# Kernel tuning notes

Measured on AMD Instinct MI355X. Metric: run time of the kernel, lower is better.

The kernel has to match this reference:

```python
import jax, jax.numpy as jnp
import numpy as np

NTOKENS = 50257
NHID = 1024
NPC = int(np.ceil(np.sqrt(NTOKENS)))            # 225 tokens per class
NCLASSES = int(np.ceil(NTOKENS / NPC))          # 224 classes
BATCH = 1024
INITRANGE = 0.1


def setup_inputs() -> dict:
    key = jax.random.key(0)
    k1, k2, k3, k4 = jax.random.split(key, 4)
    inputs = jax.random.normal(k1, (BATCH, NHID), dtype=jnp.float32)
    labels = jax.random.randint(k2, (BATCH,), 0, NTOKENS, dtype=jnp.int64)
    layer_top_W = jax.random.uniform(k3, (NHID, NCLASSES), minval=-INITRANGE, maxval=INITRANGE, dtype=jnp.float32)
    layer_top_b = jnp.zeros((NCLASSES,), dtype=jnp.float32)
    layer_bottom_W = jax.random.uniform(k4, (NCLASSES, NHID, NPC), minval=-INITRANGE, maxval=INITRANGE, dtype=jnp.float32)
    layer_bottom_b = jnp.zeros((NCLASSES, NPC), dtype=jnp.float32)
    return {
        "inputs": inputs,
        "labels": labels,
        "layer_top_W": layer_top_W,
        "layer_top_b": layer_top_b,
        "layer_bottom_W": layer_bottom_W,
        "layer_bottom_b": layer_bottom_b,
    }


def reference(inputs, labels, layer_top_W, layer_top_b, layer_bottom_W, layer_bottom_b):
    batch_size = inputs.shape[0]
    # decompose label into (class, within-class) position; old-torch `/` on Long == floor div
    pos_top = labels // NPC            # [B]
    pos_bottom = labels % NPC          # [B]

    # top-level class distribution: [B, nclasses]
    top_logits = inputs @ layer_top_W + layer_top_b
    top_probs = jax.nn.softmax(top_logits, axis=1)

    # gather per-sample class weight slices and do batched matvec:
    # layer_bottom_W[pos_top]: [B, nhid, npc]
    bottom_logits = jnp.einsum("bd,bdc->bc", inputs, layer_bottom_W[pos_top]) + layer_bottom_b[pos_top]
    bottom_probs = jax.nn.softmax(bottom_logits, axis=1)

    rows = jnp.arange(batch_size)
    target_probs = top_probs[rows, pos_top] * bottom_probs[rows, pos_bottom]  # [B]
    return target_probs
```

## Files before the change

kernel.cpp:

```cpp
#include <hip/hip_runtime.h>
#include <math.h>

#define NHID 1024
#define NPC  225
#define NCLS 224
#define BATCH 1024

#define MAX_ITEMS 352
#define N_TOP     (BATCH / 8)

#define WS_NITEMS 0
#define WS_ORDER  16
#define WS_ITEMS  2048
#define WS_PTOP   4096

__device__ __forceinline__ void group_samples(const int* __restrict__ labels,
                                              int* __restrict__ ws,
                                              float* __restrict__ smf, int tid)
{
    int* cnt   = (int*)smf;
    int* scan  = (int*)smf + 256;
    int* iscan = (int*)smf + 512;
    int* cur   = (int*)smf + 768;

    if (tid < 256) cnt[tid] = 0;
    __syncthreads();
    for (int i = tid; i < BATCH; i += 1024)
        atomicAdd(&cnt[labels[i] / NPC], 1);
    __syncthreads();

    int myc = 0, myi = 0;
    if (tid < 256) {
        myc = (tid < NCLS) ? cnt[tid] : 0;
        myi = (myc + 7) >> 3;
        scan[tid]  = myc;
        iscan[tid] = myi;
    }
    __syncthreads();
    for (int off = 1; off < 256; off <<= 1) {
        int a = 0, b = 0;
        if (tid < 256 && tid >= off) { a = scan[tid - off]; b = iscan[tid - off]; }
        __syncthreads();
        if (tid < 256) { scan[tid] += a; iscan[tid] += b; }
        __syncthreads();
    }
    if (tid < 256) {
        const int sbase = scan[tid]  - myc;
        const int ibase = iscan[tid] - myi;
        if (tid == 255) ws[WS_NITEMS] = iscan[255];
        cur[tid] = sbase;
        if (tid < NCLS) {
            for (int t = 0; t < myi; ++t) {
                int* it = ws + WS_ITEMS + 4 * (ibase + t);
                it[0] = tid;
                it[1] = sbase + 8 * t;
                it[2] = min(8, myc - 8 * t);
            }
        }
    }
    __syncthreads();
    for (int i = tid; i < BATCH; i += 1024) {
        int c = labels[i] / NPC;
        int p = atomicAdd(&cur[c], 1);
        ws[WS_ORDER + p] = i;
    }
}

__global__ __launch_bounds__(1024, 4) void k1_top(const float* __restrict__ X,
                                                  const int* __restrict__ labels,
                                                  const float* __restrict__ Wt,
                                                  const float* __restrict__ bt,
                                                  int* __restrict__ ws)
{
    __shared__ __align__(16) float sm[14848];
    const int tid  = threadIdx.x;
    const int wave = tid >> 6;
    const int lane = tid & 63;

    if (blockIdx.x == N_TOP) {
        group_samples(labels, ws, sm, tid);
        return;
    }
    const int sbase = blockIdx.x * 8;

    for (int idx = tid; idx < 2048; idx += 1024) {
        const int j  = idx & 7;
        const int d4 = idx >> 3;
        const float4 v = ((const float4*)&X[(size_t)(sbase + j) * NHID])[d4];
        float* p = &sm[48 * d4 + j];
        p[0] = v.x; p[12] = v.y; p[24] = v.z; p[36] = v.w;
    }
    __syncthreads();

    float acc[8][4];
#pragma unroll
    for (int j = 0; j < 8; ++j)
#pragma unroll
        for (int k = 0; k < 4; ++k) acc[j][k] = 0.f;

    const int c0 = lane, c1 = lane + 64, c2 = lane + 128, c3 = lane + 192;
    const bool m3 = (c3 < NCLS);
    const int d0 = wave * 64;
    const float* Wr = Wt + (size_t)d0 * NCLS;

    auto ldrow = [&](int r, float* o) {
        const float* p = Wr + (size_t)r * NCLS;
        o[0] = p[c0]; o[1] = p[c1]; o[2] = p[c2];
        o[3] = m3 ? p[c3] : 0.f;
    };
    float wbuf[4][4];
    ldrow(0, wbuf[0]); ldrow(1, wbuf[1]); ldrow(2, wbuf[2]); ldrow(3, wbuf[3]);

#pragma unroll 4
    for (int dd = 0; dd < 64; ++dd) {
        const int slot = dd & 3;
        const float cw0 = wbuf[slot][0], cw1 = wbuf[slot][1],
                    cw2 = wbuf[slot][2], cw3 = wbuf[slot][3];
        ldrow(min(dd + 4, 63), wbuf[slot]);
        const float4 a = *(const float4*)&sm[(d0 + dd) * 12 + 0];
        const float4 b = *(const float4*)&sm[(d0 + dd) * 12 + 4];
        const float xi[8] = {a.x, a.y, a.z, a.w, b.x, b.y, b.z, b.w};
#pragma unroll
        for (int j = 0; j < 8; ++j) {
            acc[j][0] = fmaf(xi[j], cw0, acc[j][0]);
            acc[j][1] = fmaf(xi[j], cw1, acc[j][1]);
            acc[j][2] = fmaf(xi[j], cw2, acc[j][2]);
            acc[j][3] = fmaf(xi[j], cw3, acc[j][3]);
        }
    }
    __syncthreads();

    float* red = sm;
    if (wave >= 8) {
#pragma unroll
        for (int j = 0; j < 8; ++j)
#pragma unroll
            for (int k = 0; k < 4; ++k) {
                int c = lane + 64 * k;
                if (c < NCLS) red[((wave - 8) * 8 + j) * 232 + c] = acc[j][k];
            }
    }
    __syncthreads();
    if (wave < 8) {
#pragma unroll
        for (int j = 0; j < 8; ++j)
#pragma unroll
            for (int k = 0; k < 4; ++k) {
                int c = lane + 64 * k;
                if (c < NCLS) red[(wave * 8 + j) * 232 + c] += acc[j][k];
            }
    }
    __syncthreads();

    if (wave < 8) {
        const int j = wave;
        const int s = sbase + j;
        float v[4];
#pragma unroll
        for (int k = 0; k < 4; ++k) {
            int c = lane + 64 * k;
            if (c < NCLS) {
                float t = bt[c];
#pragma unroll
                for (int g = 0; g < 8; ++g) t += red[(g * 8 + j) * 232 + c];
                v[k] = t;
            } else v[k] = -INFINITY;
        }
        float m = fmaxf(fmaxf(v[0], v[1]), fmaxf(v[2], v[3]));
        for (int o = 32; o > 0; o >>= 1) m = fmaxf(m, __shfl_xor(m, o));
        float e = expf(v[0] - m) + expf(v[1] - m) + expf(v[2] - m) + expf(v[3] - m);
        for (int o = 32; o > 0; o >>= 1) e += __shfl_xor(e, o);
        const int pt = labels[s] / NPC;
        if (lane == (pt & 63))
            ((float*)(ws + WS_PTOP))[s] = expf(v[pt >> 6] - m) / e;
    }
}

__global__ __launch_bounds__(1024, 4) void k2_bottom(const float* __restrict__ X,
                                                     const int* __restrict__ labels,
                                                     const float* __restrict__ Wb,
                                                     const float* __restrict__ bb,
                                                     const int* __restrict__ ws,
                                                     float* __restrict__ out)
{
    __shared__ __align__(16) float sm[14848];
    const int nitems = ws[WS_NITEMS];
    if ((int)blockIdx.x >= nitems) return;
    const int* it = ws + WS_ITEMS + 4 * blockIdx.x;
    const int cls = it[0], s0 = it[1], nt = it[2];

    const int tid  = threadIdx.x;
    const int wave = tid >> 6;
    const int lane = tid & 63;

    int s_ids[8];
#pragma unroll
    for (int j = 0; j < 8; ++j)
        s_ids[j] = (j < nt) ? ws[WS_ORDER + s0 + j] : 0;

    for (int idx = tid; idx < 2048; idx += 1024) {
        const int j  = idx & 7;
        const int d4 = idx >> 3;
        float4 v = make_float4(0.f, 0.f, 0.f, 0.f);
        if (j < nt) v = ((const float4*)&X[(size_t)s_ids[j] * NHID])[d4];
        float* p = &sm[48 * d4 + j];
        p[0] = v.x; p[12] = v.y; p[24] = v.z; p[36] = v.w;
    }
    __syncthreads();

    float acc[8][4];
#pragma unroll
    for (int j = 0; j < 8; ++j)
#pragma unroll
        for (int k = 0; k < 4; ++k) acc[j][k] = 0.f;

    const int c0 = lane, c1 = lane + 64, c2 = lane + 128, c3 = lane + 192;
    const bool m3 = (c3 < NPC);
    const int d0 = wave * 64;
    const float* Wr = Wb + (size_t)cls * (NHID * NPC) + (size_t)d0 * NPC;

    auto ldrow = [&](int r, float* o) {
        const float* p = Wr + (size_t)r * NPC;
        o[0] = __builtin_nontemporal_load(p + c0);
        o[1] = __builtin_nontemporal_load(p + c1);
        o[2] = __builtin_nontemporal_load(p + c2);
        o[3] = m3 ? __builtin_nontemporal_load(p + c3) : 0.f;
    };
    float wbuf[4][4];
    ldrow(0, wbuf[0]); ldrow(1, wbuf[1]); ldrow(2, wbuf[2]); ldrow(3, wbuf[3]);

#pragma unroll 4
    for (int dd = 0; dd < 64; ++dd) {
        const int slot = dd & 3;
        const float cw0 = wbuf[slot][0], cw1 = wbuf[slot][1],
                    cw2 = wbuf[slot][2], cw3 = wbuf[slot][3];
        ldrow(min(dd + 4, 63), wbuf[slot]);
        const float4 a = *(const float4*)&sm[(d0 + dd) * 12 + 0];
        const float4 b = *(const float4*)&sm[(d0 + dd) * 12 + 4];
        const float xi[8] = {a.x, a.y, a.z, a.w, b.x, b.y, b.z, b.w};
#pragma unroll
        for (int j = 0; j < 8; ++j) {
            acc[j][0] = fmaf(xi[j], cw0, acc[j][0]);
            acc[j][1] = fmaf(xi[j], cw1, acc[j][1]);
            acc[j][2] = fmaf(xi[j], cw2, acc[j][2]);
            acc[j][3] = fmaf(xi[j], cw3, acc[j][3]);
        }
    }
    __syncthreads();

    float* red = sm;
    if (wave >= 8) {
#pragma unroll
        for (int j = 0; j < 8; ++j)
#pragma unroll
            for (int k = 0; k < 4; ++k) {
                int c = lane + 64 * k;
                if (c < NPC) red[((wave - 8) * 8 + j) * 232 + c] = acc[j][k];
            }
    }
    __syncthreads();
    if (wave < 8) {
#pragma unroll
        for (int j = 0; j < 8; ++j)
#pragma unroll
            for (int k = 0; k < 4; ++k) {
                int c = lane + 64 * k;
                if (c < NPC) red[(wave * 8 + j) * 232 + c] += acc[j][k];
            }
    }
    __syncthreads();

    if (wave < 8) {
        const int j = wave;
        if (j < nt) {
            const int s = s_ids[j];
            float v[4];
#pragma unroll
            for (int k = 0; k < 4; ++k) {
                int c = lane + 64 * k;
                if (c < NPC) {
                    float t = bb[(size_t)cls * NPC + c];
#pragma unroll
                    for (int g = 0; g < 8; ++g) t += red[(g * 8 + j) * 232 + c];
                    v[k] = t;
                } else v[k] = -INFINITY;
            }
            float m = fmaxf(fmaxf(v[0], v[1]), fmaxf(v[2], v[3]));
            for (int o = 32; o > 0; o >>= 1) m = fmaxf(m, __shfl_xor(m, o));
            float e = expf(v[0] - m) + expf(v[1] - m) + expf(v[2] - m) + expf(v[3] - m);
            for (int o = 32; o > 0; o >>= 1) e += __shfl_xor(e, o);
            const int pb = labels[s] % NPC;
            if (lane == (pb & 63)) {
                const float pt = ((const float*)(ws + WS_PTOP))[s];
                out[s] = pt * (expf(v[pb >> 6] - m) / e);
            }
        }
    }
}

extern "C" void kernel_launch(void* const* d_in, const int* in_sizes, int n_in,
                              void* d_out, int out_size, void* d_ws, size_t ws_size,
                              hipStream_t stream)
{
    const float* X      = (const float*)d_in[0];
    const int*   labels = (const int*)  d_in[1];
    const float* Wt     = (const float*)d_in[2];
    const float* bt     = (const float*)d_in[3];
    const float* Wb     = (const float*)d_in[4];
    const float* bb     = (const float*)d_in[5];

    hipLaunchKernelGGL(k1_top, dim3(N_TOP + 1), dim3(1024), 0, stream,
                       X, labels, Wt, bt, (int*)d_ws);
    hipLaunchKernelGGL(k2_bottom, dim3(MAX_ITEMS), dim3(1024), 0, stream,
                       X, labels, Wb, bb, (const int*)d_ws, (float*)d_out);
}
```

Measured before the change: 303.7 us.

## Fuse top and per-class bottom passes into one kernel, finalize with tiny multiply

```diff
diff --git a/kernel.cpp b/kernel.cpp
--- a/kernel.cpp
+++ b/kernel.cpp
@@ -5,89 +5,152 @@
 #define NPC  225
 #define NCLS 224
 #define BATCH 1024
-
-#define MAX_ITEMS 352
-#define N_TOP     (BATCH / 8)
-
-#define WS_NITEMS 0
-#define WS_ORDER  16
-#define WS_ITEMS  2048
-#define WS_PTOP   4096
-
-__device__ __forceinline__ void group_samples(const int* __restrict__ labels,
-                                              int* __restrict__ ws,
-                                              float* __restrict__ smf, int tid)
-{
-    int* cnt   = (int*)smf;
-    int* scan  = (int*)smf + 256;
-    int* iscan = (int*)smf + 512;
-    int* cur   = (int*)smf + 768;
-
-    if (tid < 256) cnt[tid] = 0;
-    __syncthreads();
-    for (int i = tid; i < BATCH; i += 1024)
-        atomicAdd(&cnt[labels[i] / NPC], 1);
-    __syncthreads();
-
-    int myc = 0, myi = 0;
-    if (tid < 256) {
-        myc = (tid < NCLS) ? cnt[tid] : 0;
-        myi = (myc + 7) >> 3;
-        scan[tid]  = myc;
-        iscan[tid] = myi;
-    }
-    __syncthreads();
-    for (int off = 1; off < 256; off <<= 1) {
-        int a = 0, b = 0;
-        if (tid < 256 && tid >= off) { a = scan[tid - off]; b = iscan[tid - off]; }
-        __syncthreads();
-        if (tid < 256) { scan[tid] += a; iscan[tid] += b; }
-        __syncthreads();
-    }
-    if (tid < 256) {
-        const int sbase = scan[tid]  - myc;
-        const int ibase = iscan[tid] - myi;
-        if (tid == 255) ws[WS_NITEMS] = iscan[255];
-        cur[tid] = sbase;
-        if (tid < NCLS) {
-            for (int t = 0; t < myi; ++t) {
-                int* it = ws + WS_ITEMS + 4 * (ibase + t);
-                it[0] = tid;
-                it[1] = sbase + 8 * t;
-                it[2] = min(8, myc - 8 * t);
-            }
-        }
-    }
-    __syncthreads();
-    for (int i = tid; i < BATCH; i += 1024) {
-        int c = labels[i] / NPC;
-        int p = atomicAdd(&cur[c], 1);
-        ws[WS_ORDER + p] = i;
-    }
-}
-
-__global__ __launch_bounds__(1024, 4) void k1_top(const float* __restrict__ X,
-                                                  const int* __restrict__ labels,
-                                                  const float* __restrict__ Wt,
-                                                  const float* __restrict__ bt,
-                                                  int* __restrict__ ws)
+#define N_TOP (BATCH / 8)
+
+#define WS_PT 0
+#define WS_PB 1024
+
+__global__ __launch_bounds__(1024, 4) void k_fused(const float* __restrict__ X,
+                                                   const int* __restrict__ labels,
+                                                   const float* __restrict__ Wt,
+                                                   const float* __restrict__ bt,
+                                                   const float* __restrict__ Wb,
+                                                   const float* __restrict__ bb,
+                                                   float* __restrict__ ws)
 {
     __shared__ __align__(16) float sm[14848];
+    __shared__ int slist[128];
+    __shared__ int scnt;
+
     const int tid  = threadIdx.x;
     const int wave = tid >> 6;
     const int lane = tid & 63;
-
-    if (blockIdx.x == N_TOP) {
-        group_samples(labels, ws, sm, tid);
+    const int j8   = tid & 7;
+    const int t8   = tid >> 3;
+
+    if ((int)blockIdx.x < NCLS) {
+        const int cls = blockIdx.x;
+        if (tid == 0) scnt = 0;
+        __syncthreads();
+        {
+            const int lab = labels[tid];
+            if (lab / NPC == cls) {
+                const int p = atomicAdd(&scnt, 1);
+                if (p < 128) slist[p] = tid;
+            }
+        }
+        __syncthreads();
+        const int cnt = scnt;
+        if (cnt == 0) return;
+
+        const int c0 = lane, c1 = lane + 64, c2 = lane + 128, c3 = lane + 192;
+        const bool m3 = (c3 < NPC);
+        const int d0 = wave * 64;
+        const float* Wr = Wb + (size_t)cls * (NHID * NPC) + (size_t)d0 * NPC;
+
+        for (int base = 0; base < cnt; base += 8) {
+            const int nt = min(8, cnt - base);
+
+            const int sid = (j8 < nt) ? slist[base + j8] : -1;
+            for (int d4 = t8; d4 < 256; d4 += 128) {
+                float4 v = make_float4(0.f, 0.f, 0.f, 0.f);
+                if (sid >= 0) v = ((const float4*)&X[(size_t)sid * NHID])[d4];
+                float* p = &sm[48 * d4 + j8];
+                p[0] = v.x; p[12] = v.y; p[24] = v.z; p[36] = v.w;
+            }
+            __syncthreads();
+
+            float acc[8][4];
+#pragma unroll
+            for (int j = 0; j < 8; ++j)
+#pragma unroll
+                for (int k = 0; k < 4; ++k) acc[j][k] = 0.f;
+
+            auto ldrow = [&](int r, float* o) {
+                const float* p = Wr + (size_t)r * NPC;
+                o[0] = __builtin_nontemporal_load(p + c0);
+                o[1] = __builtin_nontemporal_load(p + c1);
+                o[2] = __builtin_nontemporal_load(p + c2);
+                o[3] = m3 ? __builtin_nontemporal_load(p + c3) : 0.f;
+            };
+            float wbuf[4][4];
+            ldrow(0, wbuf[0]); ldrow(1, wbuf[1]); ldrow(2, wbuf[2]); ldrow(3, wbuf[3]);
+
+#pragma unroll 4
+            for (int dd = 0; dd < 64; ++dd) {
+                const int slot = dd & 3;
+                const float cw0 = wbuf[slot][0], cw1 = wbuf[slot][1],
+                            cw2 = wbuf[slot][2], cw3 = wbuf[slot][3];
+                ldrow(min(dd + 4, 63), wbuf[slot]);
+                const float4 a = *(const float4*)&sm[(d0 + dd) * 12 + 0];
+                const float4 b = *(const float4*)&sm[(d0 + dd) * 12 + 4];
+                const float xi[8] = {a.x, a.y, a.z, a.w, b.x, b.y, b.z, b.w};
+#pragma unroll
+                for (int j = 0; j < 8; ++j) {
+                    acc[j][0] = fmaf(xi[j], cw0, acc[j][0]);
+                    acc[j][1] = fmaf(xi[j], cw1, acc[j][1]);
+                    acc[j][2] = fmaf(xi[j], cw2, acc[j][2]);
+                    acc[j][3] = fmaf(xi[j], cw3, acc[j][3]);
+                }
+            }
+            __syncthreads();
+
+            float* red = sm;
+            if (wave >= 8) {
+#pragma unroll
+                for (int j = 0; j < 8; ++j)
+#pragma unroll
+                    for (int k = 0; k < 4; ++k) {
+                        int c = lane + 64 * k;
+                        if (c < NPC) red[((wave - 8) * 8 + j) * 232 + c] = acc[j][k];
+                    }
+            }
+            __syncthreads();
+            if (wave < 8) {
+#pragma unroll
+                for (int j = 0; j < 8; ++j)
+#pragma unroll
+                    for (int k = 0; k < 4; ++k) {
+                        int c = lane + 64 * k;
+                        if (c < NPC) red[(wave * 8 + j) * 232 + c] += acc[j][k];
+                    }
+            }
+            __syncthreads();
+
+            if (wave < 8) {
+                const int j = wave;
+                if (j < nt) {
+                    const int s = slist[base + j];
+                    float v[4];
+#pragma unroll
+                    for (int k = 0; k < 4; ++k) {
+                        int c = lane + 64 * k;
+                        if (c < NPC) {
+                            float t = bb[(size_t)cls * NPC + c];
+#pragma unroll
+                            for (int g = 0; g < 8; ++g) t += red[(g * 8 + j) * 232 + c];
+                            v[k] = t;
+                        } else v[k] = -INFINITY;
+                    }
+                    float m = fmaxf(fmaxf(v[0], v[1]), fmaxf(v[2], v[3]));
+                    for (int o = 32; o > 0; o >>= 1) m = fmaxf(m, __shfl_xor(m, o));
+                    float e = expf(v[0] - m) + expf(v[1] - m) + expf(v[2] - m) + expf(v[3] - m);
+                    for (int o = 32; o > 0; o >>= 1) e += __shfl_xor(e, o);
+                    const int pb = labels[s] % NPC;
+                    if (lane == (pb & 63))
+                        ws[WS_PB + s] = expf(v[pb >> 6] - m) / e;
+                }
+            }
+            __syncthreads();
+        }
         return;
     }
-    const int sbase = blockIdx.x * 8;
-
-    for (int idx = tid; idx < 2048; idx += 1024) {
-        const int j  = idx & 7;
-        const int d4 = idx >> 3;
-        const float4 v = ((const float4*)&X[(size_t)(sbase + j) * NHID])[d4];
-        float* p = &sm[48 * d4 + j];
+
+    const int sbase = (blockIdx.x - NCLS) * 8;
+
+    for (int d4 = t8; d4 < 256; d4 += 128) {
+        const float4 v = ((const float4*)&X[(size_t)(sbase + j8) * NHID])[d4];
+        float* p = &sm[48 * d4 + j8];
         p[0] = v.x; p[12] = v.y; p[24] = v.z; p[36] = v.w;
     }
     __syncthreads();
@@ -172,130 +235,14 @@
         for (int o = 32; o > 0; o >>= 1) e += __shfl_xor(e, o);
         const int pt = labels[s] / NPC;
         if (lane == (pt & 63))
-            ((float*)(ws + WS_PTOP))[s] = expf(v[pt >> 6] - m) / e;
+            ws[WS_PT + s] = expf(v[pt >> 6] - m) / e;
     }
 }
 
-__global__ __launch_bounds__(1024, 4) void k2_bottom(const float* __restrict__ X,
-                                                     const int* __restrict__ labels,
-                                                     const float* __restrict__ Wb,
-                                                     const float* __restrict__ bb,
-                                                     const int* __restrict__ ws,
-                                                     float* __restrict__ out)
+__global__ void k_mul(const float* __restrict__ ws, float* __restrict__ out)
 {
-    __shared__ __align__(16) float sm[14848];
-    const int nitems = ws[WS_NITEMS];
-    if ((int)blockIdx.x >= nitems) return;
-    const int* it = ws + WS_ITEMS + 4 * blockIdx.x;
-    const int cls = it[0], s0 = it[1], nt = it[2];
-
-    const int tid  = threadIdx.x;
-    const int wave = tid >> 6;
-    const int lane = tid & 63;
-
-    int s_ids[8];
-#pragma unroll
-    for (int j = 0; j < 8; ++j)
-        s_ids[j] = (j < nt) ? ws[WS_ORDER + s0 + j] : 0;
-
-    for (int idx = tid; idx < 2048; idx += 1024) {
-        const int j  = idx & 7;
-        const int d4 = idx >> 3;
-        float4 v = make_float4(0.f, 0.f, 0.f, 0.f);
-        if (j < nt) v = ((const float4*)&X[(size_t)s_ids[j] * NHID])[d4];
-        float* p = &sm[48 * d4 + j];
-        p[0] = v.x; p[12] = v.y; p[24] = v.z; p[36] = v.w;
-    }
-    __syncthreads();
-
-    float acc[8][4];
-#pragma unroll
-    for (int j = 0; j < 8; ++j)
-#pragma unroll
-        for (int k = 0; k < 4; ++k) acc[j][k] = 0.f;
-
-    const int c0 = lane, c1 = lane + 64, c2 = lane + 128, c3 = lane + 192;
-    const bool m3 = (c3 < NPC);
-    const int d0 = wave * 64;
-    const float* Wr = Wb + (size_t)cls * (NHID * NPC) + (size_t)d0 * NPC;
-
-    auto ldrow = [&](int r, float* o) {
-        const float* p = Wr + (size_t)r * NPC;
-        o[0] = __builtin_nontemporal_load(p + c0);
-        o[1] = __builtin_nontemporal_load(p + c1);
-        o[2] = __builtin_nontemporal_load(p + c2);
-        o[3] = m3 ? __builtin_nontemporal_load(p + c3) : 0.f;
-    };
-    float wbuf[4][4];
-    ldrow(0, wbuf[0]); ldrow(1, wbuf[1]); ldrow(2, wbuf[2]); ldrow(3, wbuf[3]);
-
-#pragma unroll 4
-    for (int dd = 0; dd < 64; ++dd) {
-        const int slot = dd & 3;
-        const float cw0 = wbuf[slot][0], cw1 = wbuf[slot][1],
-                    cw2 = wbuf[slot][2], cw3 = wbuf[slot][3];
-        ldrow(min(dd + 4, 63), wbuf[slot]);
-        const float4 a = *(const float4*)&sm[(d0 + dd) * 12 + 0];
-        const float4 b = *(const float4*)&sm[(d0 + dd) * 12 + 4];
-        const float xi[8] = {a.x, a.y, a.z, a.w, b.x, b.y, b.z, b.w};
-#pragma unroll
-        for (int j = 0; j < 8; ++j) {
-            acc[j][0] = fmaf(xi[j], cw0, acc[j][0]);
-            acc[j][1] = fmaf(xi[j], cw1, acc[j][1]);
-            acc[j][2] = fmaf(xi[j], cw2, acc[j][2]);
-            acc[j][3] = fmaf(xi[j], cw3, acc[j][3]);
-        }
-    }
-    __syncthreads();
-
-    float* red = sm;
-    if (wave >= 8) {
-#pragma unroll
-        for (int j = 0; j < 8; ++j)
-#pragma unroll
-            for (int k = 0; k < 4; ++k) {
-                int c = lane + 64 * k;
-                if (c < NPC) red[((wave - 8) * 8 + j) * 232 + c] = acc[j][k];
-            }
-    }
-    __syncthreads();
-    if (wave < 8) {
-#pragma unroll
-        for (int j = 0; j < 8; ++j)
-#pragma unroll
-            for (int k = 0; k < 4; ++k) {
-                int c = lane + 64 * k;
-                if (c < NPC) red[(wave * 8 + j) * 232 + c] += acc[j][k];
-            }
-    }
-    __syncthreads();
-
-    if (wave < 8) {
-        const int j = wave;
-        if (j < nt) {
-            const int s = s_ids[j];
-            float v[4];
-#pragma unroll
-            for (int k = 0; k < 4; ++k) {
-                int c = lane + 64 * k;
-                if (c < NPC) {
-                    float t = bb[(size_t)cls * NPC + c];
-#pragma unroll
-                    for (int g = 0; g < 8; ++g) t += red[(g * 8 + j) * 232 + c];
-                    v[k] = t;
-                } else v[k] = -INFINITY;
-            }
-            float m = fmaxf(fmaxf(v[0], v[1]), fmaxf(v[2], v[3]));
-            for (int o = 32; o > 0; o >>= 1) m = fmaxf(m, __shfl_xor(m, o));
-            float e = expf(v[0] - m) + expf(v[1] - m) + expf(v[2] - m) + expf(v[3] - m);
-            for (int o = 32; o > 0; o >>= 1) e += __shfl_xor(e, o);
-            const int pb = labels[s] % NPC;
-            if (lane == (pb & 63)) {
-                const float pt = ((const float*)(ws + WS_PTOP))[s];
-                out[s] = pt * (expf(v[pb >> 6] - m) / e);
-            }
-        }
-    }
+    const int i = blockIdx.x * 256 + threadIdx.x;
+    if (i < BATCH) out[i] = ws[WS_PT + i] * ws[WS_PB + i];
 }
 
 extern "C" void kernel_launch(void* const* d_in, const int* in_sizes, int n_in,
@@ -309,8 +256,8 @@
     const float* Wb     = (const float*)d_in[4];
     const float* bb     = (const float*)d_in[5];
 
-    hipLaunchKernelGGL(k1_top, dim3(N_TOP + 1), dim3(1024), 0, stream,
-                       X, labels, Wt, bt, (int*)d_ws);
-    hipLaunchKernelGGL(k2_bottom, dim3(MAX_ITEMS), dim3(1024), 0, stream,
-                       X, labels, Wb, bb, (const int*)d_ws, (float*)d_out);
+    hipLaunchKernelGGL(k_fused, dim3(NCLS + N_TOP), dim3(1024), 0, stream,
+                       X, labels, Wt, bt, Wb, bb, (float*)d_ws);
+    hipLaunchKernelGGL(k_mul, dim3(BATCH / 256), dim3(256), 0, stream,
+                       (const float*)d_ws, (float*)d_out);
 }
```

Result: slower. 345.8 us (+13.9%).
